# Kernel tuning notes

Measured on AMD Instinct MI355X. Metric: run time of the kernel, lower is better.

Reference implementation:

```python
import jax, jax.numpy as jnp
import numpy as np

# ---- static config (mirrors CE defaults) ----
PS = 7        # patch size
WS = 27       # search window (per side)
S0 = 4        # query stride (stride0)
KS = 100      # k_s: top-k kept by search
KA = 100      # k_a: top-k used for aggregation
SCALE = 10.0  # softmax_scale
CI = 16       # inter_channels


def conv2d(x, w, b, pad):
    y = jax.lax.conv_general_dilated(
        x, w, (1, 1), [(pad, pad), (pad, pad)],
        dimension_numbers=("NCHW", "OIHW", "NCHW"))
    return y + b[None, :, None, None]


def all_patches(v):
    """[T,C,H,W] -> [T, H*W, C*PS*PS]; top-left anchored PSxPS patches,
    edge-clamped at the border (dnls-style bounded patch extraction)."""
    t, c, h, w = v.shape
    ii = jnp.clip(jnp.arange(h)[:, None] + jnp.arange(PS)[None, :], 0, h - 1)
    jj = jnp.clip(jnp.arange(w)[:, None] + jnp.arange(PS)[None, :], 0, w - 1)
    p = v[:, :, ii][:, :, :, :, jj]          # [T,C,H,PS,W,PS]
    p = p.transpose(0, 2, 4, 1, 3, 5)        # [T,H,W,C,PS,PS]
    return p.reshape(t, h * w, c * PS * PS)


def setup_inputs():
    key = jax.random.key(0)
    ks = jax.random.split(key, 4)
    vid = jax.random.normal(ks[0], (4, 64, 128, 128), jnp.float32)
    g_w = jax.random.normal(ks[1], (CI, 64, 3, 3), jnp.float32) * 0.05
    g_b = jnp.zeros((CI,), jnp.float32)
    theta_w = jax.random.normal(ks[2], (CI, 64, 1, 1), jnp.float32) * 0.1
    theta_b = jnp.zeros((CI,), jnp.float32)
    return {"vid": vid, "g_w": g_w, "g_b": g_b,
            "theta_w": theta_w, "theta_b": theta_b}


def reference(vid, g_w, g_b, theta_w, theta_b):
    t, c, h, w = vid.shape
    nH, nW = h // S0, w // S0
    Q, N = nH * nW, h * w

    # feature extraction (g -> search features, theta -> aggregation values)
    v1 = conv2d(vid, g_w, g_b, 1)          # [T,CI,H,W]
    v2 = conv2d(vid, theta_w, theta_b, 0)  # [T,CI,H,W]

    # windowed k-NN patch search: query grid (stride0) vs all keys (stride1=1)
    P1 = all_patches(v1)                                    # [T,N,D]
    qis = jnp.arange(nH) * S0
    qjs = jnp.arange(nW) * S0
    qflat = (qis[:, None] * w + qjs[None, :]).reshape(-1)   # [Q]
    Pq = P1[:, qflat]                                       # [T,Q,D]
    scores = jnp.einsum("tqd,tnd->tqn", Pq, P1)             # [T,Q,N]

    off = jnp.arange(WS) - WS // 2
    ci = jnp.clip(qis[:, None] + off, 0, h - 1)             # [nH,WS]
    cj = jnp.clip(qjs[:, None] + off, 0, w - 1)             # [nW,WS]
    cand = (ci[:, None, :, None] * w + cj[None, :, None, :]).reshape(Q, WS * WS)
    dists = jnp.take_along_axis(scores, cand[None], axis=2)  # [T,Q,WS*WS]

    d_k, widx = jax.lax.top_k(dists, KS)                    # [T,Q,KS]
    inds = jnp.take_along_axis(jnp.broadcast_to(cand[None], dists.shape),
                               widx, axis=2)                # flat key positions

    # top-k softmax aggregation weights
    wgt = jax.nn.softmax(d_k[..., :KA] * SCALE, axis=-1)    # [T,Q,KA]
    inds_a = inds[..., :KA]

    # wpsum: weighted sum of value patches gathered at neighbor indices,
    # expressed as sparse-scatter matrix @ dense patch matrix
    A = jnp.zeros((t, Q, N), scores.dtype).at[
        jnp.arange(t)[:, None, None],
        jnp.arange(Q)[None, :, None],
        inds_a].add(wgt)                                    # [T,Q,N]
    P2 = all_patches(v2)                                    # [T,N,D]
    z = jnp.einsum("tqn,tnd->tqd", A, P2)                   # [T,Q,CI*PS*PS]

    # ifold: scatter-add overlapping patches + count normalization
    z = z.reshape(t, Q, CI, PS, PS).transpose(0, 2, 1, 3, 4)
    z = z.reshape(t, CI, Q * PS * PS)
    ri = jnp.clip(qis[:, None] + jnp.arange(PS), 0, h - 1)  # [nH,PS]
    rj = jnp.clip(qjs[:, None] + jnp.arange(PS), 0, w - 1)  # [nW,PS]
    pix = (ri[:, None, :, None] * w + rj[None, :, None, :]).reshape(-1)
    Y = jnp.zeros((t, CI, N), z.dtype).at[:, :, pix].add(z)
    Zc = jnp.zeros((N,), z.dtype).at[pix].add(1.0)
    y = (Y / Zc).reshape(t, CI, h, w)
    return y
```

## Files before the change

kernel.cpp:

```cpp
#include <hip/hip_runtime.h>
#include <hip/hip_bf16.h>

#define T_ 4
#define C_ 64
#define H_ 128
#define W_ 128
#define CI_ 16
#define PS_ 7
#define NC_ 729
#define S0_ 4
#define KS_ 100
#define NQ_ 1024
#define SCALE_ 10.0f
#define HW_ (H_*W_)
#define RW_ 45
#define LCAP_ 768
#define CB_ 8

typedef float v2f __attribute__((ext_vector_type(2)));
#if __has_builtin(__builtin_elementwise_fma)
#define VFMA(a, b, c) __builtin_elementwise_fma((a), (b), (c))
#else
#define VFMA(a, b, c) ((a) * (b) + (c))
#endif

__device__ __forceinline__ float4 colfix(float4 r, bool loB, bool hiB) {
  float4 o;
  o.x = loB ? 0.f : (hiB ? r.y : r.x);
  o.y = loB ? r.x : (hiB ? r.z : r.y);
  o.z = loB ? r.y : (hiB ? r.w : r.z);
  o.w = loB ? r.z : (hiB ? 0.f : r.w);
  return o;
}

__global__ __launch_bounds__(128, 1) void conv3x3_kernel(
    const float* __restrict__ vid, const float* __restrict__ gw,
    const float* __restrict__ gb, float4* __restrict__ v1cs) {
  __shared__ float wls[C_ * 9 * 4];
  const int tid = threadIdx.x;
  const int g = blockIdx.y, t = blockIdx.z;
  for (int m = tid; m < C_ * 9 * 4; m += 128) {
    int co = m & 3, ck = m >> 2;
    wls[m] = gw[((size_t)(g * 4 + co) * C_) * 9 + ck];
  }
  __syncthreads();
  const int ti0 = (blockIdx.x >> 3) * 16, tj0 = (blockIdx.x & 7) * 16;
  const int u = tid >> 3, v = tid & 7;
  const int i = ti0 + u, j0 = tj0 + 2 * v;
  const int c0 = j0 - 1;
  const int c0c = min(max(c0, 0), W_ - 4);
  const bool loB = (c0 < 0), hiB = (c0 > W_ - 4);
  const int rm1 = max(i - 1, 0), rp1 = min(i + 1, H_ - 1);
  const float mk0 = (i > 0) ? 1.f : 0.f;
  const float mk2 = (i < H_ - 1) ? 1.f : 0.f;
  const int o0 = rm1 * W_ + c0c, o1 = i * W_ + c0c, o2 = rp1 * W_ + c0c;

  float accA[4], accB[4];
#pragma unroll
  for (int co = 0; co < 4; ++co) { accA[co] = gb[g * 4 + co]; accB[co] = gb[g * 4 + co]; }

  const float* vb = vid + ((size_t)t * C_) * HW_;
#pragma unroll 1
  for (int cb = 0; cb < C_; cb += CB_) {
    float4 r[CB_][3];
#pragma unroll
    for (int c = 0; c < CB_; ++c) {
      const float* p = vb + (size_t)(cb + c) * HW_;
      r[c][0] = *(const float4*)(p + o0);
      r[c][1] = *(const float4*)(p + o1);
      r[c][2] = *(const float4*)(p + o2);
    }
#pragma unroll
    for (int c = 0; c < CB_; ++c) {
      float4 f0 = colfix(r[c][0], loB, hiB);
      float4 f1 = colfix(r[c][1], loB, hiB);
      float4 f2 = colfix(r[c][2], loB, hiB);
      f0.x *= mk0; f0.y *= mk0; f0.z *= mk0; f0.w *= mk0;
      f2.x *= mk2; f2.y *= mk2; f2.z *= mk2; f2.w *= mk2;
      const float* wc = &wls[(cb + c) * 36];
      float e0[4] = {f0.x, f0.y, f0.z, f0.w};
      float e1[4] = {f1.x, f1.y, f1.z, f1.w};
      float e2[4] = {f2.x, f2.y, f2.z, f2.w};
#pragma unroll
      for (int kj = 0; kj < 3; ++kj) {
#pragma unroll
        for (int co = 0; co < 4; ++co) {
          accA[co] = fmaf(wc[(0 * 3 + kj) * 4 + co], e0[kj],     accA[co]);
          accB[co] = fmaf(wc[(0 * 3 + kj) * 4 + co], e0[kj + 1], accB[co]);
          accA[co] = fmaf(wc[(1 * 3 + kj) * 4 + co], e1[kj],     accA[co]);
          accB[co] = fmaf(wc[(1 * 3 + kj) * 4 + co], e1[kj + 1], accB[co]);
          accA[co] = fmaf(wc[(2 * 3 + kj) * 4 + co], e2[kj],     accA[co]);
          accB[co] = fmaf(wc[(2 * 3 + kj) * 4 + co], e2[kj + 1], accB[co]);
        }
      }
    }
  }
  const size_t o = ((size_t)g * T_ + t) * HW_ + i * W_ + j0;
  v1cs[o]     = make_float4(accA[0], accA[1], accA[2], accA[3]);
  v1cs[o + 1] = make_float4(accB[0], accB[1], accB[2], accB[3]);
}

__global__ __launch_bounds__(256, 1) void conv1x1_kernel(
    const float* __restrict__ vid, const float* __restrict__ tw,
    const float* __restrict__ tb, float4* __restrict__ v2cs) {
  __shared__ float w[C_ * 4];
  const int t = blockIdx.y, cc = blockIdx.z;
  for (int m = threadIdx.x; m < C_ * 4; m += 256) {
    int o = m & 3, c = m >> 2;
    w[m] = tw[(cc * 4 + o) * C_ + c];
  }
  __syncthreads();
  const int pix = blockIdx.x * 256 + threadIdx.x;
  float acc[4];
#pragma unroll
  for (int o = 0; o < 4; ++o) acc[o] = tb[cc * 4 + o];
  const float* vb = vid + ((size_t)t * C_) * HW_ + pix;
#pragma unroll 1
  for (int c0 = 0; c0 < C_; c0 += 16) {
    float x[16];
#pragma unroll
    for (int uu = 0; uu < 16; ++uu) x[uu] = vb[(size_t)(c0 + uu) * HW_];
#pragma unroll
    for (int uu = 0; uu < 16; ++uu)
#pragma unroll
      for (int o = 0; o < 4; ++o)
        acc[o] = fmaf(w[(c0 + uu) * 4 + o], x[uu], acc[o]);
  }
  v2cs[((size_t)cc * T_ + t) * HW_ + pix] = make_float4(acc[0], acc[1], acc[2], acc[3]);
}

__global__ __launch_bounds__(1024) void dist_kernel(
    const float4* __restrict__ v1cs, float* __restrict__ distG) {
  __shared__ float4 Rs[RW_ * RW_];
  const int tid = threadIdx.x;
  const int t = blockIdx.y;
  const int qi0 = (blockIdx.x >> 3) * 16, qj0 = (blockIdx.x & 7) * 16;
  const int w = tid >> 6, lane = tid & 63;
  const int di = (w >> 2) * 4, dj = (w & 3) * 4;
  const int qi = qi0 + di, qj = qj0 + dj;
  const int a_lo = max(13 - qi, 0), b_lo = max(13 - qj, 0);
  const int ai = lane >> 1, bg = lane & 1;
  const bool active = ai < 27;
  const int a = min(a_lo + ai, 26);
  const int bs = bg ? 13 : b_lo;

  v2f acc2[14];
#pragma unroll
  for (int j = 0; j < 14; ++j) acc2[j] = (v2f){0.f, 0.f};

#pragma unroll 1
  for (int cc = 0; cc < 4; ++cc) {
    __syncthreads();
    const float4* src = v1cs + ((size_t)cc * T_ + t) * HW_;
    for (int p = tid; p < RW_ * RW_; p += 1024) {
      int uu = p / RW_, vv = p - uu * RW_;
      int row = min(max(qi0 - 13 + uu, 0), H_ - 1);
      int col = min(max(qj0 - 13 + vv, 0), W_ - 1);
      Rs[p] = src[row * W_ + col];
    }
    __syncthreads();
    if (active) {
#pragma unroll 1
      for (int r = 0; r < 7; ++r) {
        v2f qlo[7], qhi[7];
        const float4* qrow = &Rs[(di + 13 + r) * RW_ + dj + 13];
#pragma unroll
        for (int s = 0; s < 7; ++s) {
          float4 qq = qrow[s];
          qlo[s] = (v2f){qq.x, qq.y};
          qhi[s] = (v2f){qq.z, qq.w};
        }
        const float4* crow = &Rs[(di + a + r) * RW_ + dj + bs];
#pragma unroll
        for (int y = 0; y < 20; ++y) {
          float4 vv = crow[y];
          v2f vlo = (v2f){vv.x, vv.y}, vhi = (v2f){vv.z, vv.w};
          const int s_lo = (y > 13) ? (y - 13) : 0;
          const int s_hi = (y < 6) ? y : 6;
#pragma unroll
          for (int s = s_lo; s <= s_hi; ++s) {
            int j = y - s;
            acc2[j] = VFMA(qlo[s], vlo, acc2[j]);
            acc2[j] = VFMA(qhi[s], vhi, acc2[j]);
          }
        }
      }
    }
  }
  if (active) {
    const int q = ((qi >> 2) << 5) + (qj >> 2);
    float* out = distG + ((size_t)t * NQ_ + q) * NC_ + a * 27 + bs;
#pragma unroll
    for (int j = 0; j < 14; ++j) out[j] = acc2[j].x + acc2[j].y;
  }
}

__global__ __launch_bounds__(256) void select_kernel(
    const float* __restrict__ distG, int* __restrict__ sel_n,
    float* __restrict__ sel_w, float* __restrict__ wsum_out) {
  __shared__ float dist[NC_];
  __shared__ unsigned int ukey[NC_];
  __shared__ float redf[4];
  __shared__ unsigned int hist[256];
  __shared__ int lk[LCAP_];
  __shared__ unsigned int lkey[LCAP_];
  __shared__ unsigned int scal[6];

  const int tid = threadIdx.x;
  const int lane = tid & 63, wid = tid >> 6;
  const int q = blockIdx.x, t = blockIdx.y;
  const int qi = (q >> 5) * S0_, qj = (q & 31) * S0_;
  const int a_lo = max(13 - qi, 0), b_lo = max(13 - qj, 0);
  const size_t base = ((size_t)t * NQ_ + q) * NC_;

  for (int h = tid; h < 256; h += 256) hist[h] = 0;
  if (tid == 0) { scal[2] = 0; scal[3] = 0; }
  float lmax = -INFINITY;
  for (int k = tid; k < NC_; k += 256) {
    int aa = k / 27, bb = k - aa * 27;
    int kk = max(aa, a_lo) * 27 + max(bb, b_lo);
    float d = distG[base + kk];
    dist[k] = d;
    unsigned int u = __float_as_uint(d);
    ukey[k] = u ^ (((unsigned int)((int)u >> 31)) | 0x80000000u);
    lmax = fmaxf(lmax, d);
  }
#pragma unroll
  for (int off = 32; off > 0; off >>= 1)
    lmax = fmaxf(lmax, __shfl_down(lmax, off, 64));
  if (lane == 0) redf[wid] = lmax;
  __syncthreads();
  const float dmax = fmaxf(fmaxf(redf[0], redf[1]), fmaxf(redf[2], redf[3]));
  for (int k = tid; k < NC_; k += 256) atomicAdd(&hist[ukey[k] >> 24], 1u);
  __syncthreads();
  if (wid == 0) {
    int s4 = (int)(hist[lane * 4] + hist[lane * 4 + 1] + hist[lane * 4 + 2] + hist[lane * 4 + 3]);
    int s = s4;
#pragma unroll
    for (int off = 1; off < 64; off <<= 1) {
      int o = __shfl_down(s, off, 64);
      if (lane + off < 64) s += o;
    }
    int above = s - s4;
    if (above < KS_ && s >= KS_) {
      int run = above;
#pragma unroll
      for (int bb = 3; bb >= 0; --bb) {
        int h = (int)hist[lane * 4 + bb];
        if (run + h >= KS_) { scal[0] = (unsigned int)(lane * 4 + bb); scal[1] = (unsigned int)run; break; }
        run += h;
      }
    }
  }
  __syncthreads();
  const unsigned int beta = scal[0];
  const int run = (int)scal[1];
  for (int h = tid; h < 256; h += 256) hist[h] = 0;
  __syncthreads();
  for (int k = tid; k < NC_; k += 256)
    if ((ukey[k] >> 24) == beta) atomicAdd(&hist[(ukey[k] >> 16) & 0xFFu], 1u);
  __syncthreads();
  if (wid == 0) {
    int s4 = (int)(hist[lane * 4] + hist[lane * 4 + 1] + hist[lane * 4 + 2] + hist[lane * 4 + 3]);
    int s = s4;
#pragma unroll
    for (int off = 1; off < 64; off <<= 1) {
      int o = __shfl_down(s, off, 64);
      if (lane + off < 64) s += o;
    }
    int above = run + s - s4;
    if (above < KS_ && run + s >= KS_) {
      int r2 = above;
#pragma unroll
      for (int bb = 3; bb >= 0; --bb) {
        int h = (int)hist[lane * 4 + bb];
        if (r2 + h >= KS_) { scal[4] = (unsigned int)(lane * 4 + bb); scal[5] = (unsigned int)r2; break; }
        r2 += h;
      }
    }
  }
  __syncthreads();
  const unsigned int beta2 = scal[4];
  const int run2 = (int)scal[5];
  const size_t outb = ((size_t)t * NQ_ + q) * KS_;
  float lsum = 0.f;
  for (int k = tid; k < NC_; k += 256) {
    unsigned int key = ukey[k];
    unsigned int bin = key >> 24;
    bool sel = false, bdry = false;
    if (bin > beta) sel = true;
    else if (bin == beta) {
      unsigned int b2 = (key >> 16) & 0xFFu;
      if (b2 > beta2) sel = true;
      else if (b2 == beta2) bdry = true;
    }
    if (sel) {
      unsigned int slot = atomicAdd(&scal[2], 1u);
      int aa = k / 27, bb = k - aa * 27;
      int ni = min(max(qi + aa - 13, 0), H_ - 1);
      int nj = min(max(qj + bb - 13, 0), W_ - 1);
      float wv = __expf(SCALE_ * (dist[k] - dmax));
      sel_n[outb + slot] = (ni << 7) | nj;
      sel_w[outb + slot] = wv;
      lsum += wv;
    } else if (bdry) {
      unsigned int pos = atomicAdd(&scal[3], 1u);
      if (pos < LCAP_) { lk[pos] = k; lkey[pos] = key; }
    }
  }
  __syncthreads();
  const int L = min((int)scal[3], LCAP_);
  for (int i = tid; i < L; i += 256) {
    unsigned int key = lkey[i];
    int k = lk[i];
    int cnt = run2;
    for (int m = 0; m < L; ++m)
      cnt += (int)((lkey[m] > key) || (lkey[m] == key && lk[m] < k));
    if (cnt < KS_) {
      unsigned int slot = atomicAdd(&scal[2], 1u);
      int aa = k / 27, bb = k - aa * 27;
      int ni = min(max(qi + aa - 13, 0), H_ - 1);
      int nj = min(max(qj + bb - 13, 0), W_ - 1);
      float wv = __expf(SCALE_ * (dist[k] - dmax));
      sel_n[outb + slot] = (ni << 7) | nj;
      sel_w[outb + slot] = wv;
      lsum += wv;
    }
  }
#pragma unroll
  for (int off = 32; off > 0; off >>= 1) lsum += __shfl_down(lsum, off, 64);
  __syncthreads();
  if (lane == 0) redf[wid] = lsum;
  __syncthreads();
  if (tid == 0) wsum_out[t * NQ_ + q] = (redf[0] + redf[1]) + (redf[2] + redf[3]);
}

__global__ __launch_bounds__(1024) void agg_kernel(
    const float4* __restrict__ v2cs, const int* __restrict__ sel_n,
    const float* __restrict__ sel_w, const float* __restrict__ wsum,
    float* __restrict__ Y) {
  __shared__ float4 Rs[RW_ * RW_];
  __shared__ int s_off[16][KS_];
  __shared__ float s_w[16][KS_];
  const int tid = threadIdx.x;
  const int t = blockIdx.y;
  const int qi0 = (blockIdx.x >> 3) * 16, qj0 = (blockIdx.x & 7) * 16;
  const int w = tid >> 6, lane = tid & 63;
  const int di = (w >> 2) * 4, dj = (w & 3) * 4;
  const int qi = qi0 + di, qj = qj0 + dj;
  const int q = ((qi >> 2) << 5) + (qj >> 2);
  const size_t base = ((size_t)t * NQ_ + q) * KS_;
  const float inv = 1.0f / wsum[t * NQ_ + q];
  for (int k = lane; k < KS_; k += 64) {
    int n = sel_n[base + k];
    int ni = n >> 7, nj = n & 127;
    s_off[w][k] = (ni - qi0 + 13) * RW_ + (nj - qj0 + 13);
    s_w[w][k] = sel_w[base + k] * inv;
  }
  const int r = lane / 7, s = lane - r * 7;
  const int myo = r * RW_ + s;
  const int oi = min(qi + r, H_ - 1), oj = min(qj + s, W_ - 1);
#pragma unroll 1
  for (int cc = 0; cc < 4; ++cc) {
    __syncthreads();
    const float4* src = v2cs + ((size_t)cc * T_ + t) * HW_;
    for (int p = tid; p < RW_ * RW_; p += 1024) {
      int uu = p / RW_, vv = p - uu * RW_;
      int row = min(max(qi0 - 13 + uu, 0), H_ - 1);
      int col = min(max(qj0 - 13 + vv, 0), W_ - 1);
      Rs[p] = src[row * W_ + col];
    }
    __syncthreads();
    if (lane < 49) {
      float4 acc = make_float4(0.f, 0.f, 0.f, 0.f);
#pragma unroll 4
      for (int k = 0; k < KS_; ++k) {
        float wv = s_w[w][k];
        float4 v = Rs[s_off[w][k] + myo];
        acc.x = fmaf(wv, v.x, acc.x);
        acc.y = fmaf(wv, v.y, acc.y);
        acc.z = fmaf(wv, v.z, acc.z);
        acc.w = fmaf(wv, v.w, acc.w);
      }
      float* yb = Y + (((size_t)t * CI_ + cc * 4) * H_ + oi) * W_ + oj;
      atomicAdd(yb, acc.x);
      atomicAdd(yb + HW_, acc.y);
      atomicAdd(yb + 2 * HW_, acc.z);
      atomicAdd(yb + 3 * HW_, acc.w);
    }
  }
}

__device__ __forceinline__ int cov_axis(int x) {
  int c = 0;
#pragma unroll
  for (int r = 0; r < 7; ++r) {
    if (x < H_ - 1) {
      int qb = x - r;
      c += (qb >= 0 && (qb & 3) == 0) ? 1 : 0;
    } else {
      c += (r >= 3) ? 1 : 0;
    }
  }
  return c;
}

__global__ void norm_kernel(float* __restrict__ Y) {
  int idx = blockIdx.x * blockDim.x + threadIdx.x;
  if (idx >= T_ * CI_ * HW_) return;
  int p = idx & (HW_ - 1);
  float z = (float)(cov_axis(p >> 7) * cov_axis(p & 127));
  Y[idx] /= z;
}

extern "C" void kernel_launch(void* const* d_in, const int* in_sizes, int n_in,
                              void* d_out, int out_size, void* d_ws, size_t ws_size,
                              hipStream_t stream) {
  const float* vid     = (const float*)d_in[0];
  const float* g_w     = (const float*)d_in[1];
  const float* g_b     = (const float*)d_in[2];
  const float* theta_w = (const float*)d_in[3];
  const float* theta_b = (const float*)d_in[4];
  float* Y = (float*)d_out;

  float* v1cs  = (float*)d_ws;
  float* v2cs  = v1cs + (size_t)4 * T_ * HW_ * 4;
  float* distG = v2cs + (size_t)4 * T_ * HW_ * 4;
  int*   sel_n = (int*)(distG + (size_t)T_ * NQ_ * NC_);
  float* sel_w = (float*)(sel_n + (size_t)T_ * NQ_ * KS_);
  float* wsumv = sel_w + (size_t)T_ * NQ_ * KS_;

  hipMemsetAsync(Y, 0, (size_t)out_size * sizeof(float), stream);

  conv3x3_kernel<<<dim3(64, 4, T_), 128, 0, stream>>>(vid, g_w, g_b, (float4*)v1cs);
  conv1x1_kernel<<<dim3(HW_ / 256, T_, 4), 256, 0, stream>>>(vid, theta_w, theta_b, (float4*)v2cs);
  dist_kernel<<<dim3(64, T_), 1024, 0, stream>>>((const float4*)v1cs, distG);
  select_kernel<<<dim3(NQ_, T_), 256, 0, stream>>>(distG, sel_n, sel_w, wsumv);
  agg_kernel<<<dim3(64, T_), 1024, 0, stream>>>((const float4*)v2cs, sel_n, sel_w, wsumv, Y);
  norm_kernel<<<(T_ * CI_ * HW_ + 255) / 256, 256, 0, stream>>>(Y);
}
```

Baseline: 263.1 us.

## Compute two query rows per wave in dist kernel with double-buffered LDS staging

Each wave now handles two vertically adjacent queries, 4 rows apart, that share the same candidate-row loads. This halves the block size to 512 threads with 31 candidate rows per lane, so every LDS candidate read feeds twice as many FMAs. The channel-chunk staging is also double-buffered: the next chunk's global loads go into registers while the current chunk is computed, which removes one barrier per iteration. The cost is more registers (two accumulator sets) and a larger LDS footprint (2x2048 float4), which may limit occupancy.

After: 263.9 us. Within noise of the previous version (+0.3%).

```diff
diff --git a/kernel.cpp b/kernel.cpp
--- a/kernel.cpp
+++ b/kernel.cpp
@@ -129,69 +129,103 @@
   v2cs[((size_t)cc * T_ + t) * HW_ + pix] = make_float4(acc[0], acc[1], acc[2], acc[3]);
 }
 
-__global__ __launch_bounds__(1024) void dist_kernel(
+__global__ __launch_bounds__(512, 2) void dist_kernel(
     const float4* __restrict__ v1cs, float* __restrict__ distG) {
-  __shared__ float4 Rs[RW_ * RW_];
+  __shared__ float4 Rs[2][2048];
   const int tid = threadIdx.x;
   const int t = blockIdx.y;
   const int qi0 = (blockIdx.x >> 3) * 16, qj0 = (blockIdx.x & 7) * 16;
   const int w = tid >> 6, lane = tid & 63;
-  const int di = (w >> 2) * 4, dj = (w & 3) * 4;
-  const int qi = qi0 + di, qj = qj0 + dj;
-  const int a_lo = max(13 - qi, 0), b_lo = max(13 - qj, 0);
-  const int ai = lane >> 1, bg = lane & 1;
-  const bool active = ai < 27;
-  const int a = min(a_lo + ai, 26);
+  const int pr = w >> 2, dj = (w & 3) * 4;
+  const int rbase = 8 * pr;
+  const int qi_p = qi0 + rbase;
+  const int qj = qj0 + dj;
+  const int la = lane >> 1, bg = lane & 1;
+  const int b_lo = max(13 - qj, 0);
   const int bs = bg ? 13 : b_lo;
-
-  v2f acc2[14];
-#pragma unroll
-  for (int j = 0; j < 14; ++j) acc2[j] = (v2f){0.f, 0.f};
-
+  const int a_lo0 = max(13 - qi_p, 0);
+  const int a_lo1 = max(9 - qi_p, 0);
+  const bool compute_ok = (la < 31);
+
+  int soff[4];
+#pragma unroll
+  for (int k = 0; k < 4; ++k) {
+    int p = min(tid + 512 * k, RW_ * RW_ - 1);
+    int uu = p / RW_, vv = p - uu * RW_;
+    int row = min(max(qi0 - 13 + uu, 0), H_ - 1);
+    int col = min(max(qj0 - 13 + vv, 0), W_ - 1);
+    soff[k] = row * W_ + col;
+  }
+
+  v2f acc0[14], acc1[14];
+#pragma unroll
+  for (int j = 0; j < 14; ++j) { acc0[j] = (v2f){0.f, 0.f}; acc1[j] = (v2f){0.f, 0.f}; }
+
+  float4 st[4];
+  {
+    const float4* src = v1cs + ((size_t)0 * T_ + t) * HW_;
+#pragma unroll
+    for (int k = 0; k < 4; ++k) st[k] = src[soff[k]];
+  }
+  int cur = 0;
 #pragma unroll 1
   for (int cc = 0; cc < 4; ++cc) {
+    float4* buf = &Rs[cur][0];
+#pragma unroll
+    for (int k = 0; k < 4; ++k) buf[tid + 512 * k] = st[k];
+    if (cc < 3) {
+      const float4* src = v1cs + ((size_t)(cc + 1) * T_ + t) * HW_;
+#pragma unroll
+      for (int k = 0; k < 4; ++k) st[k] = src[soff[k]];
+    }
     __syncthreads();
-    const float4* src = v1cs + ((size_t)cc * T_ + t) * HW_;
-    for (int p = tid; p < RW_ * RW_; p += 1024) {
-      int uu = p / RW_, vv = p - uu * RW_;
-      int row = min(max(qi0 - 13 + uu, 0), H_ - 1);
-      int col = min(max(qj0 - 13 + vv, 0), W_ - 1);
-      Rs[p] = src[row * W_ + col];
-    }
-    __syncthreads();
-    if (active) {
+    if (compute_ok) {
 #pragma unroll 1
       for (int r = 0; r < 7; ++r) {
-        v2f qlo[7], qhi[7];
-        const float4* qrow = &Rs[(di + 13 + r) * RW_ + dj + 13];
+        v2f q0lo[7], q0hi[7], q1lo[7], q1hi[7];
+        const float4* q0row = &buf[(rbase + 13 + r) * RW_ + dj + 13];
 #pragma unroll
         for (int s = 0; s < 7; ++s) {
-          float4 qq = qrow[s];
-          qlo[s] = (v2f){qq.x, qq.y};
-          qhi[s] = (v2f){qq.z, qq.w};
+          float4 qq = q0row[s];
+          q0lo[s] = (v2f){qq.x, qq.y};
+          q0hi[s] = (v2f){qq.z, qq.w};
+          float4 q2 = q0row[4 * RW_ + s];
+          q1lo[s] = (v2f){q2.x, q2.y};
+          q1hi[s] = (v2f){q2.z, q2.w};
         }
-        const float4* crow = &Rs[(di + a + r) * RW_ + dj + bs];
+        const float4* crow = &buf[(rbase + la + r) * RW_ + dj + bs];
 #pragma unroll
         for (int y = 0; y < 20; ++y) {
-          float4 vv = crow[y];
-          v2f vlo = (v2f){vv.x, vv.y}, vhi = (v2f){vv.z, vv.w};
+          float4 vv4 = crow[y];
+          v2f vlo = (v2f){vv4.x, vv4.y}, vhi = (v2f){vv4.z, vv4.w};
           const int s_lo = (y > 13) ? (y - 13) : 0;
           const int s_hi = (y < 6) ? y : 6;
 #pragma unroll
           for (int s = s_lo; s <= s_hi; ++s) {
             int j = y - s;
-            acc2[j] = VFMA(qlo[s], vlo, acc2[j]);
-            acc2[j] = VFMA(qhi[s], vhi, acc2[j]);
+            acc0[j] = VFMA(q0lo[s], vlo, acc0[j]);
+            acc0[j] = VFMA(q0hi[s], vhi, acc0[j]);
+            acc1[j] = VFMA(q1lo[s], vlo, acc1[j]);
+            acc1[j] = VFMA(q1hi[s], vhi, acc1[j]);
           }
         }
       }
     }
-  }
-  if (active) {
-    const int q = ((qi >> 2) << 5) + (qj >> 2);
-    float* out = distG + ((size_t)t * NQ_ + q) * NC_ + a * 27 + bs;
-#pragma unroll
-    for (int j = 0; j < 14; ++j) out[j] = acc2[j].x + acc2[j].y;
+    cur ^= 1;
+  }
+  if (compute_ok) {
+    const int q0q = ((qi_p >> 2) << 5) + (qj >> 2);
+    if (la >= a_lo0 && la <= 26) {
+      float* out = distG + ((size_t)t * NQ_ + q0q) * NC_ + la * 27 + bs;
+#pragma unroll
+      for (int j = 0; j < 14; ++j) out[j] = acc0[j].x + acc0[j].y;
+    }
+    const int a1 = la - 4;
+    if (a1 >= a_lo1 && a1 <= 26) {
+      float* out = distG + ((size_t)t * NQ_ + (q0q + 32)) * NC_ + a1 * 27 + bs;
+#pragma unroll
+      for (int j = 0; j < 14; ++j) out[j] = acc1[j].x + acc1[j].y;
+    }
   }
 }
 
@@ -434,7 +468,7 @@
 
   conv3x3_kernel<<<dim3(64, 4, T_), 128, 0, stream>>>(vid, g_w, g_b, (float4*)v1cs);
   conv1x1_kernel<<<dim3(HW_ / 256, T_, 4), 256, 0, stream>>>(vid, theta_w, theta_b, (float4*)v2cs);
-  dist_kernel<<<dim3(64, T_), 1024, 0, stream>>>((const float4*)v1cs, distG);
+  dist_kernel<<<dim3(64, T_), 512, 0, stream>>>((const float4*)v1cs, distG);
   select_kernel<<<dim3(NQ_, T_), 256, 0, stream>>>(distG, sel_n, sel_w, wsumv);
   agg_kernel<<<dim3(64, T_), 1024, 0, stream>>>((const float4*)v2cs, sel_n, sel_w, wsumv, Y);
   norm_kernel<<<(T_ * CI_ * HW_ + 255) / 256, 256, 0, stream>>>(Y);
```
